# Performance work log

Hardware: AMD Instinct MI355X
Metric: run time of the kernel (lower is better)

Reference implementation:

```python
import jax, jax.numpy as jnp
import numpy as np
from jax import lax

DATA_NUM, CNUM, AUG_NUM, LNUM = 64, 6, 4, 3
B, H, W = 16, 512, 512
T_SEL = 0  # fixed aug selection (torch draws np.random.randint at runtime)
EPS = 1e-8
DN = ('NCHW', 'OIHW', 'NCHW')


def setup_inputs() -> dict:
    key = jax.random.key(0)
    ks = jax.random.split(key, 8)
    GLA_img_aug = jax.random.uniform(ks[0], (B, 1, H, W), dtype=jnp.float32)
    lbl = jax.random.randint(ks[1], (B, H, W), 0, CNUM, dtype=jnp.int32)
    index = jax.random.randint(ks[2], (B,), 0, DATA_NUM, dtype=jnp.int32)
    # learned params: Bezier control params (5+2=7 slots, only 0..3 used) and per-(sample,class,aug,layer) tiny conv pairs
    param = jax.random.uniform(ks[3], (DATA_NUM, CNUM, AUG_NUM, LNUM, 7), dtype=jnp.float32)
    w1 = 0.1 * jax.random.normal(ks[4], (DATA_NUM, CNUM, AUG_NUM, LNUM, 4, 1, 3, 3), dtype=jnp.float32)
    b1 = 0.01 * jax.random.normal(ks[5], (DATA_NUM, CNUM, AUG_NUM, LNUM, 4), dtype=jnp.float32)
    w2 = 0.1 * jax.random.normal(ks[6], (DATA_NUM, CNUM, AUG_NUM, LNUM, 1, 4, 3, 3), dtype=jnp.float32)
    b2 = 0.01 * jax.random.normal(ks[7], (DATA_NUM, CNUM, AUG_NUM, LNUM, 1), dtype=jnp.float32)
    return {"GLA_img_aug": GLA_img_aug, "lbl": lbl, "index": index,
            "param": param, "w1": w1, "b1": b1, "w2": w2, "b2": b2}


def _conv_pair(x, w1, b1, w2, b2):
    # x: [1,H,W]; per-sample Conv2d(1,4,3,p=1) -> Conv2d(4,1,3,p=1)
    y = lax.conv_general_dilated(x[None], w1, (1, 1), 'SAME', dimension_numbers=DN) + b1[None, :, None, None]
    y = lax.conv_general_dilated(y, w2, (1, 1), 'SAME', dimension_numbers=DN) + b2[None, :, None, None]
    return y[0]

_conv_batch = jax.vmap(_conv_pair)  # batched over per-sample weights


def _ftransfer(xn, lbl, i, index, param, w1, b1, w2, b2):
    raw = xn                                   # [B,1,H,W]
    mask = (lbl[:, None, :, :] == i)           # [B,1,H,W]
    c = xn * mask
    pp = jax.nn.sigmoid(param[index, i, T_SEL])   # [B,L,7]  (p := sigmoid)
    W1, B1 = w1[index, i, T_SEL], b1[index, i, T_SEL]
    W2, B2 = w2[index, i, T_SEL], b2[index, i, T_SEL]
    for layer in range(LNUM):
        p1 = pp[:, layer, 0][:, None, None, None]
        p2 = pp[:, layer, 1][:, None, None, None]
        p1v = pp[:, layer, 2][:, None, None, None]
        p2v = pp[:, layer, 3][:, None, None, None]
        mix = jax.nn.sigmoid(_conv_batch(raw, W1[:, layer], B1[:, layer], W2[:, layer], B2[:, layer]))
        om = 1.0 - c
        ct = 3.0 * om**2 * c * p1 + 3.0 * om * c**2 * p2 + c**3          # p0=0,  p3=1
        cv = om**3 + 3.0 * om**2 * c * p1v + 3.0 * om * c**2 * p2v       # p0v=1, p3v=0
        c = jnp.clip(ct * mix + cv * (1.0 - mix), 0.0, 1.0)
    # write back only where label == i (equivalent to torch's flag-filtered scatter)
    return jnp.where(mask, c, raw)


def reference(GLA_img_aug, lbl, index, param, w1, b1, w2, b2):
    x = GLA_img_aug
    mn = jnp.min(x, axis=(1, 2, 3), keepdims=True)
    mx = jnp.max(x, axis=(1, 2, 3), keepdims=True)
    scale = mx - mn + EPS
    xn = (x - mn) / scale
    for i in range(CNUM):
        xn = _ftransfer(xn, lbl, i, index, param, w1, b1, w2, b2)
    return xn * scale + mn
```

## Files before the change

kernel.cpp:

```cpp
#include <hip/hip_runtime.h>
#include <stdint.h>

#define HW 512
#define IMG (HW*HW)
#define CNUM_ 6

#define TILE 64
#define HALO 12
#define ST 88
#define SSTR 89
#define NT 512
#define RCAP 256

typedef float f2 __attribute__((ext_vector_type(2)));

#define LTOT 3840

#define RECBASE 2048
#define REC_F 96
#define VARBASE (RECBASE + 96*REC_F)
#define VAR_F 27

__global__ __launch_bounds__(256) void k_prep(const float4* __restrict__ x4,
                       const int* __restrict__ index, const float* __restrict__ param,
                       const float* __restrict__ w1, const float* __restrict__ b1,
                       const float* __restrict__ w2, const float* __restrict__ b2,
                       float* __restrict__ wsf){
    __shared__ float w1s[108], w2s[108], b1s[12], b2s[3], prm[21];
    __shared__ float smn[4], smx[4];
    const int r = blockIdx.x, t = threadIdx.x;
    if (r >= 96){
        int blk = r - 96;
        int base4 = blk * 1024;
        float vmin = 1e30f, vmax = -1e30f;
#pragma unroll
        for (int k = 0; k < 4; k++){
            float4 v = x4[base4 + k*256 + t];
            vmin = fminf(vmin, fminf(fminf(v.x, v.y), fminf(v.z, v.w)));
            vmax = fmaxf(vmax, fmaxf(fmaxf(v.x, v.y), fmaxf(v.z, v.w)));
        }
#pragma unroll
        for (int off = 32; off > 0; off >>= 1){
            vmin = fminf(vmin, __shfl_down(vmin, off));
            vmax = fmaxf(vmax, __shfl_down(vmax, off));
        }
        int wv = t >> 6;
        if ((t & 63) == 0){ smn[wv] = vmin; smx[wv] = vmax; }
        __syncthreads();
        if (t == 0){
            wsf[2*blk]     = fminf(fminf(smn[0], smn[1]), fminf(smn[2], smn[3]));
            wsf[2*blk + 1] = fmaxf(fmaxf(smx[0], smx[1]), fmaxf(smx[2], smx[3]));
        }
        return;
    }
    const int b = r / 6, i = r % 6;
    const int lb0 = (index[b]*CNUM_ + i) * 12;
    if (t < 108){
        int l = t / 36, j = t % 36;
        w1s[t] = w1[(lb0 + l)*36 + j];
        w2s[t] = w2[(lb0 + l)*36 + j];
    }
    if (t < 12) b1s[t] = b1[(lb0 + t/4)*4 + (t%4)];
    if (t < 3)  b2s[t] = b2[lb0 + t];
    if (t < 21) prm[t] = param[(lb0 + t/7)*7 + (t%7)];
    __syncthreads();
    float* rec = wsf + RECBASE + r*REC_F;
    float* var = wsf + VARBASE + r*9*3*VAR_F;
    for (int u = t; u < 9*3*26; u += 256){
        int kind = u / 78, rem = u % 78, l = rem / 26, e = rem % 26;
        int rowk = kind / 3, colk = kind % 3;
        if (e < 25){
            int ty = e/5 - 2, tx = e%5 - 2;
            float we = 0.f;
            for (int d = 0; d < 9; d++){
                int dy = d/3 - 1, dx = d%3 - 1;
                if ((rowk==0 && dy<0)||(rowk==2 && dy>0)||(colk==0 && dx<0)||(colk==2 && dx>0)) continue;
                int ey = ty - dy, ex = tx - dx;
                if (ey < -1 || ey > 1 || ex < -1 || ex > 1) continue;
                for (int c = 0; c < 4; c++)
                    we += w2s[l*36 + c*9 + d] * w1s[l*36 + c*9 + (ey+1)*3 + (ex+1)];
            }
            var[(kind*3 + l)*VAR_F + e] = we;
            if (kind == 4) rec[l*25 + e] = we;
        } else {
            float be = b2s[l];
            for (int c = 0; c < 4; c++){
                float sw = 0.f;
                for (int d = 0; d < 9; d++){
                    int dy = d/3 - 1, dx = d%3 - 1;
                    if ((rowk==0 && dy<0)||(rowk==2 && dy>0)||(colk==0 && dx<0)||(colk==2 && dx>0)) continue;
                    sw += w2s[l*36 + c*9 + d];
                }
                be += b1s[l*4 + c] * sw;
            }
            var[(kind*3 + l)*VAR_F + 25] = be;
            if (kind == 4) rec[75 + l] = be;
        }
    }
    if (t < 18){
        int l = t / 6, q = t % 6;
        float p1  = __builtin_amdgcn_rcpf(1.f + __expf(-prm[l*7 + 0]));
        float p2  = __builtin_amdgcn_rcpf(1.f + __expf(-prm[l*7 + 1]));
        float p1v = __builtin_amdgcn_rcpf(1.f + __expf(-prm[l*7 + 2]));
        float p2v = __builtin_amdgcn_rcpf(1.f + __expf(-prm[l*7 + 3]));
        float v;
        switch (q){
            case 0: v = 3.f*p1; break;
            case 1: v = 3.f*p2 - 6.f*p1; break;
            case 2: v = 1.f + 3.f*p1 - 3.f*p2; break;
            case 3: v = 3.f*p1v - 3.f; break;
            case 4: v = 3.f - 6.f*p1v + 3.f*p2v; break;
            default: v = -1.f + 3.f*p1v - 3.f*p2v; break;
        }
        rec[78 + l*6 + q] = v;
    }
}

__device__ __forceinline__ float sig1(float z){
    return __builtin_amdgcn_rcpf(1.f + __expf(-z));
}

__device__ __forceinline__ float bez3(float c, float mix, const float* __restrict__ cf){
    float ct = c * (cf[0] + c * (cf[1] + c * cf[2]));
    float cv = 1.f + c * (cf[3] + c * (cf[4] + c * cf[5]));
    float r = cv + mix * (ct - cv);
    return __builtin_amdgcn_fmed3f(r, 0.f, 1.f);
}

__device__ __forceinline__ f2 splat(float v){ f2 r = {v, v}; return r; }

__device__ __forceinline__ f2 sig2(f2 z){
    f2 r;
    r.x = __builtin_amdgcn_rcpf(1.f + __expf(-z.x));
    r.y = __builtin_amdgcn_rcpf(1.f + __expf(-z.y));
    return r;
}

__device__ __forceinline__ f2 bez3p(f2 c, f2 mix, const float* __restrict__ cf){
    f2 ct = c * (splat(cf[0]) + c * (splat(cf[1]) + c * splat(cf[2])));
    f2 cv = splat(1.f) + c * (splat(cf[3]) + c * (splat(cf[4]) + c * splat(cf[5])));
    f2 r = cv + mix * (ct - cv);
    r.x = __builtin_amdgcn_fmed3f(r.x, 0.f, 1.f);
    r.y = __builtin_amdgcn_fmed3f(r.y, 0.f, 1.f);
    return r;
}

__device__ __forceinline__ void load_taps(const float* __restrict__ s, int pos, float* tp){
    const float* sp0 = s + pos - (2*SSTR + 2);
    const float* sp1 = s + pos + (SSTR - 2);
#pragma unroll
    for (int wy = 0; wy < 3; wy++)
#pragma unroll
    for (int wx = 0; wx < 5; wx++)
        tp[wy*5 + wx] = sp0[wy*SSTR + wx];
#pragma unroll
    for (int wy = 0; wy < 2; wy++)
#pragma unroll
    for (int wx = 0; wx < 5; wx++)
        tp[15 + wy*5 + wx] = sp1[wy*SSTR + wx];
}

__device__ __forceinline__ void conv_px(const float* __restrict__ s, int pos,
                                        const float* __restrict__ rec,
                                        float& z0, float& z1, float& z2, float& cc){
    float tp[25];
    load_taps(s, pos, tp);
    f2 a0 = {rec[75], 0.f};
    f2 a1 = {rec[76], 0.f};
    f2 a2 = {rec[77], 0.f};
#pragma unroll
    for (int e = 0; e < 24; e += 2){
        f2 tv = {tp[e], tp[e+1]};
        f2 w0 = {rec[e],      rec[e+1]};
        f2 w1 = {rec[25 + e], rec[26 + e]};
        f2 w2 = {rec[50 + e], rec[51 + e]};
        a0 += w0 * tv;
        a1 += w1 * tv;
        a2 += w2 * tv;
    }
    float t24 = tp[24];
    z0 = a0.x + a0.y + rec[24]*t24;
    z1 = a1.x + a1.y + rec[49]*t24;
    z2 = a2.x + a2.y + rec[74]*t24;
    cc = tp[12];
}

__device__ __forceinline__ unsigned short* gl_addr(float* out, int sbase, int Y0, int X0, int e){
    return (unsigned short*)(out + sbase + (Y0 + HALO + (e >> 7))*HW + X0 + HALO) + (e & 127);
}

__device__ __forceinline__ void classify_px(int ce, unsigned short pos, int lane,
        int* cnt, unsigned short* lst, float* out, int sbase, int Y0, int X0){
    unsigned long long m0 = __ballot(ce & 1);
    unsigned long long m1 = __ballot(ce & 2);
    unsigned long long m2 = __ballot(ce & 4);
    int basev = 0;
    if (lane < 6){
        unsigned long long mc = ((lane & 1) ? m0 : ~m0)
                              & ((lane & 2) ? m1 : ~m1)
                              & ((lane & 4) ? m2 : ~m2);
        int pc = __popcll(mc);
        if (pc) basev = atomicAdd(&cnt[lane], pc);
    }
    int mybase = __shfl(basev, ce < 6 ? ce : 0);
    if (ce < 6){
        unsigned long long mself = ((ce & 1) ? m0 : ~m0)
                                 & ((ce & 2) ? m1 : ~m1)
                                 & ((ce & 4) ? m2 : ~m2);
        int p = mybase + __popcll(mself & ((1ull << lane) - 1ull));
        if (ce < 3){
            int capc = 1408 - (ce << 7);
            int offc = ce * (1472 - (ce << 6));
            if (p < capc) lst[offc + p] = pos;
        } else {
            int d = ce - 3;
            int capc = 1056 - 96*d;
            int offc = d * (1104 - 48*d);
            if (p < capc) *gl_addr(out, sbase, Y0, X0, offc + p) = pos;
        }
    }
}

__global__ __launch_bounds__(NT, 8) void k_main(
        const float* __restrict__ x, const int* __restrict__ lbl,
        float* __restrict__ out, const float* __restrict__ wsf){
    __shared__ float s[ST*SSTR];
    __shared__ unsigned short lst[LTOT];
    __shared__ unsigned rlst[RCAP];
    __shared__ int cnt[8];
    __shared__ float snorm[4];
    const int lin = ((blockIdx.z << 3) + blockIdx.y) * 8 + blockIdx.x;
    const int tile = ((lin & 7) << 7) + (lin >> 3);
    const int bz = tile >> 6, by = (tile >> 3) & 7, bx = tile & 7;
    const int b = bz;
    const int X0 = bx * TILE - HALO, Y0 = by * TILE - HALO;
    const int tid = threadIdx.x;
    const int lane = tid & 63;
    const int sbase = b * IMG;
    const bool edgeblk = (bx == 0) | (bx == 7) | (by == 0) | (by == 7);

    if (tid < 8) cnt[tid] = 0;
    if (tid < 64){
        float pmn = wsf[2*(b*64 + tid)];
        float pmx = wsf[2*(b*64 + tid) + 1];
#pragma unroll
        for (int off = 32; off > 0; off >>= 1){
            pmn = fminf(pmn, __shfl_down(pmn, off));
            pmx = fmaxf(pmx, __shfl_down(pmx, off));
        }
        if (tid == 0){
            float scv = pmx - pmn + 1e-8f;
            snorm[0] = pmn; snorm[1] = scv; snorm[2] = 1.0f / scv;
        }
    }
    __syncthreads();
    const float mn = snorm[0], sc = snorm[1], inv = snorm[2];
    const float mninv = mn * inv;

    if (!edgeblk){
        int q = tid << 2;
        int ly = q / ST, lx = q - ly*ST;
        int pbase = ly*SSTR + lx;
        for (int it = 0; it < 4; it++){
            bool act = (it < 3) | (tid < (ST*ST - 3*4*NT) / 4);
            float4 xv = {0.f, 0.f, 0.f, 0.f};
            int4  lv = {255, 255, 255, 255};
            if (act){
                int off = sbase + ((Y0 + ly) << 9) + (X0 + lx);
                xv = *(const float4*)(x + off);
                lv = *(const int4*)(lbl + off);
                s[pbase + 0] = xv.x*inv - mninv;
                s[pbase + 1] = xv.y*inv - mninv;
                s[pbase + 2] = xv.z*inv - mninv;
                s[pbase + 3] = xv.w*inv - mninv;
            }
            int mrow = min(ly, ST-1-ly);
#pragma unroll
            for (int j = 0; j < 4; j++){
                int c = (&lv.x)[j];
                int lxj = lx + j;
                int margin = min(min(lxj, ST-1-lxj), mrow);
                int ce = 7;
                if (act && c < CNUM_ && margin >= 2 + 2*c) ce = c;
                classify_px(ce, (unsigned short)(pbase + j), lane, cnt, lst, out, sbase, Y0, X0);
            }
            lx += 24; ly += 23; pbase += 23*SSTR + 24;
            if (lx >= ST){ lx -= ST; ly += 1; pbase += SSTR - ST; }
        }
    } else {
        int ly = tid / ST, lx = tid % ST;
        int pos = ly*SSTR + lx;
        for (int it = 0; it < 16; it++){
            bool inb = ly < ST;
            int gy = Y0 + ly, gx = X0 + lx;
            bool valid = inb && (unsigned)gy < (unsigned)HW && (unsigned)gx < (unsigned)HW;
            float v = 0.f; int c = 255;
            if (valid){
                int off = sbase + (gy << 9) + gx;
                v = x[off]*inv - mninv;
                c = lbl[off];
            }
            if (inb) s[pos] = v;
            int margin = min(min(lx, ST-1-lx), min(ly, ST-1-ly));
            bool ring = valid && ((gx==0) | (gx==HW-1) | (gy==0) | (gy==HW-1));
            bool mainok = valid && !ring && c < CNUM_ && margin >= 2 + 2*c;
            int ce = mainok ? c : 7;
            classify_px(ce, (unsigned short)pos, lane, cnt, lst, out, sbase, Y0, X0);
            {
                bool ringok = ring && c < CNUM_ && margin >= 2;
                unsigned long long rm = __ballot(ringok);
                if (rm){
                    int base = 0;
                    if (lane == 0) base = atomicAdd(&cnt[6], __popcll(rm));
                    base = __shfl(base, 0);
                    if (ringok){
                        int p = base + __popcll(rm & ((1ull << lane) - 1ull));
                        if (p < RCAP) rlst[p] = ((unsigned)c << 16) | (unsigned)pos;
                    }
                }
            }
            lx += 72; ly += 5; pos += 517;
            if (lx >= ST){ lx -= ST; ly += 1; pos += 1; }
        }
    }
    __syncthreads();
    const int rn = min(cnt[6], RCAP);

    unsigned short pf[9];
#pragma unroll
    for (int d = 0; d < 3; d++){
        int capc = 1056 - 96*d;
        int offc = d * (1104 - 48*d);
        int nB = min(cnt[3 + d], capc);
#pragma unroll
        for (int sl = 0; sl < 3; sl++){
            int j = tid + sl*NT;
            unsigned short pv = 0;
            if (j < nB) pv = *gl_addr(out, sbase, Y0, X0, offc + j);
            pf[d*3 + sl] = pv;
        }
    }

#pragma unroll
    for (int cls = 0; cls < CNUM_; cls++){
        const int capc = (cls < 3) ? (1408 - (cls << 7)) : (1056 - 96*(cls - 3));
        const float* rec = wsf + RECBASE + (b*CNUM_ + cls)*REC_F;
        const int n = min(cnt[cls], capc);
        const int j0 = tid, j1 = tid + NT, j2 = tid + 2*NT;
        const bool v0 = j0 < n, v1 = j1 < n, v2 = j2 < n;
        int p0 = 0, p1 = 0, p2 = 0;
        if (cls < 3){
            const unsigned short* lp = lst + cls * (1472 - (cls << 6));
            if (v0) p0 = lp[j0];
            if (v1) p1 = lp[j1];
            if (v2) p2 = lp[j2];
        } else {
            p0 = pf[(cls-3)*3 + 0];
            p1 = pf[(cls-3)*3 + 1];
            p2 = pf[(cls-3)*3 + 2];
        }
        __builtin_amdgcn_s_setprio(1);
        float z00=0.f, z01=0.f, z02=0.f, cc0=0.f;
        float z10=0.f, z11=0.f, z12=0.f, cc1=0.f;
        float u0, u1, u2;
        if (v0) conv_px(s, p0, rec, z00, z01, z02, cc0);
        if (v1) conv_px(s, p1, rec, z10, z11, z12, cc1);
        if (v0 | v1){
            f2 cP = {cc0, cc1};
            cP = bez3p(cP, sig2((f2){z00, z10}), rec + 78);
            cP = bez3p(cP, sig2((f2){z01, z11}), rec + 84);
            cP = bez3p(cP, sig2((f2){z02, z12}), rec + 90);
            u0 = cP.x; u1 = cP.y;
        }
        if (v2){
            float za, zb, zc, cc;
            conv_px(s, p2, rec, za, zb, zc, cc);
            cc = bez3(cc, sig1(za), rec + 78);
            cc = bez3(cc, sig1(zb), rec + 84);
            u2 = bez3(cc, sig1(zc), rec + 90);
        }
        __builtin_amdgcn_s_setprio(0);
        int hav = -1; float rupd = 0.f;
        if (edgeblk && tid < rn){
            unsigned e = rlst[tid];
            int rc = (int)(e >> 16), pos = (int)(e & 0xffff);
            int ly = pos / SSTR, lx = pos % SSTR;
            int margin = min(min(lx, ST-1-lx), min(ly, ST-1-ly));
            if (rc == cls && margin >= 2 + 2*cls){
                int gy = Y0 + ly, gx = X0 + lx;
                int rowk = (gy == 0) ? 0 : ((gy == HW-1) ? 2 : 1);
                int colk = (gx == 0) ? 0 : ((gx == HW-1) ? 2 : 1);
                const float* vb = wsf + VARBASE + ((b*CNUM_ + cls)*9 + rowk*3 + colk)*3*VAR_F;
                float tp[25];
                load_taps(s, pos, tp);
                float c = tp[12];
#pragma unroll
                for (int l = 0; l < 3; l++){
                    float z = vb[l*VAR_F + 25];
#pragma unroll
                    for (int e2 = 0; e2 < 25; e2++) z += vb[l*VAR_F + e2] * tp[e2];
                    c = bez3(c, sig1(z), rec + 78 + 6*l);
                }
                rupd = c; hav = pos;
            }
        }
        __syncthreads();
        if (v0) s[p0] = u0;
        if (v1) s[p1] = u1;
        if (v2) s[p2] = u2;
        if (hav >= 0) s[hav] = rupd;
        __syncthreads();
    }

    for (int j = tid; j < TILE*TILE; j += NT){
        int py = j >> 6, px = j & 63;
        int gy = Y0 + HALO + py, gx = X0 + HALO + px;
        out[sbase + gy*HW + gx] = s[(HALO + py)*SSTR + (HALO + px)] * sc + mn;
    }
}

extern "C" void kernel_launch(void* const* d_in, const int* in_sizes, int n_in,
                              void* d_out, int out_size, void* d_ws, size_t ws_size,
                              hipStream_t stream){
    const float* x     = (const float*)d_in[0];
    const int*   lbl   = (const int*)  d_in[1];
    const int*   index = (const int*)  d_in[2];
    const float* param = (const float*)d_in[3];
    const float* w1    = (const float*)d_in[4];
    const float* b1    = (const float*)d_in[5];
    const float* w2    = (const float*)d_in[6];
    const float* b2    = (const float*)d_in[7];
    float* out = (float*)d_out;
    float* wsf = (float*)d_ws;

    k_prep<<<1120, 256, 0, stream>>>((const float4*)x, index, param, w1, b1, w2, b2, wsf);
    dim3 g(8, 8, 16);
    k_main<<<g, NT, 0, stream>>>(x, lbl, out, wsf);
}
```

Baseline: 165.8 us.

## Remap tiles so each XCD owns two images; vectorize edge-block loads

The block-to-tile mapping is rewritten so each XCD (lin&7) handles two whole images, and edge tiles are scheduled first, before interior tiles. This is meant to improve L2 locality of halo reads and to balance the slower edge blocks. Edge blocks now share the float4/int4 vectorized load path with interior blocks, using per-quad bounds checks in place of the scalar 16-iteration loop. The risk is that quads straddling the image boundary rely on X0 alignment to be handled correctly.

```diff
diff --git a/kernel.cpp b/kernel.cpp
--- a/kernel.cpp
+++ b/kernel.cpp
@@ -230,9 +230,20 @@
     __shared__ int cnt[8];
     __shared__ float snorm[4];
     const int lin = ((blockIdx.z << 3) + blockIdx.y) * 8 + blockIdx.x;
-    const int tile = ((lin & 7) << 7) + (lin >> 3);
-    const int bz = tile >> 6, by = (tile >> 3) & 7, bx = tile & 7;
-    const int b = bz;
+    const int xcd = lin & 7;
+    const int e = lin >> 3;
+    int img2, idx;
+    if (e < 56){
+        int r = e >> 1; img2 = e & 1;
+        if (r < 8)       idx = r;
+        else if (r < 16) idx = 56 + (r - 8);
+        else { int t = r - 16; idx = (1 + (t >> 1))*8 + (t & 1)*7; }
+    } else {
+        int f = e - 56; img2 = f & 1; int t = f >> 1;
+        idx = (1 + t/6)*8 + 1 + t%6;
+    }
+    const int b = xcd*2 + img2;
+    const int by = idx >> 3, bx = idx & 7;
     const int X0 = bx * TILE - HALO, Y0 = by * TILE - HALO;
     const int tid = threadIdx.x;
     const int lane = tid & 63;
@@ -257,22 +268,30 @@
     const float mn = snorm[0], sc = snorm[1], inv = snorm[2];
     const float mninv = mn * inv;
 
-    if (!edgeblk){
+    {
         int q = tid << 2;
         int ly = q / ST, lx = q - ly*ST;
         int pbase = ly*SSTR + lx;
         for (int it = 0; it < 4; it++){
             bool act = (it < 3) | (tid < (ST*ST - 3*4*NT) / 4);
+            int gy = Y0 + ly, gxb = X0 + lx;
+            bool vq = act & ((unsigned)gy < (unsigned)HW) & ((unsigned)gxb <= (unsigned)(HW - 4));
             float4 xv = {0.f, 0.f, 0.f, 0.f};
             int4  lv = {255, 255, 255, 255};
-            if (act){
-                int off = sbase + ((Y0 + ly) << 9) + (X0 + lx);
+            if (vq){
+                int off = sbase + (gy << 9) + gxb;
                 xv = *(const float4*)(x + off);
                 lv = *(const int4*)(lbl + off);
-                s[pbase + 0] = xv.x*inv - mninv;
-                s[pbase + 1] = xv.y*inv - mninv;
-                s[pbase + 2] = xv.z*inv - mninv;
-                s[pbase + 3] = xv.w*inv - mninv;
+                xv.x = xv.x*inv - mninv;
+                xv.y = xv.y*inv - mninv;
+                xv.z = xv.z*inv - mninv;
+                xv.w = xv.w*inv - mninv;
+            }
+            if (act){
+                s[pbase + 0] = xv.x;
+                s[pbase + 1] = xv.y;
+                s[pbase + 2] = xv.z;
+                s[pbase + 3] = xv.w;
             }
             int mrow = min(ly, ST-1-ly);
 #pragma unroll
@@ -280,47 +299,29 @@
                 int c = (&lv.x)[j];
                 int lxj = lx + j;
                 int margin = min(min(lxj, ST-1-lxj), mrow);
-                int ce = 7;
-                if (act && c < CNUM_ && margin >= 2 + 2*c) ce = c;
+                bool ringj = false;
+                if (edgeblk){
+                    int gxj = gxb + j;
+                    ringj = vq & ((gxj==0) | (gxj==HW-1) | (gy==0) | (gy==HW-1));
+                }
+                int ce = (c < CNUM_ && !ringj && margin >= 2 + 2*c) ? c : 7;
                 classify_px(ce, (unsigned short)(pbase + j), lane, cnt, lst, out, sbase, Y0, X0);
+                if (edgeblk){
+                    bool ringok = ringj && c < CNUM_ && margin >= 2;
+                    unsigned long long rm = __ballot(ringok);
+                    if (rm){
+                        int base = 0;
+                        if (lane == 0) base = atomicAdd(&cnt[6], __popcll(rm));
+                        base = __shfl(base, 0);
+                        if (ringok){
+                            int p = base + __popcll(rm & ((1ull << lane) - 1ull));
+                            if (p < RCAP) rlst[p] = ((unsigned)c << 16) | (unsigned)(pbase + j);
+                        }
+                    }
+                }
             }
             lx += 24; ly += 23; pbase += 23*SSTR + 24;
             if (lx >= ST){ lx -= ST; ly += 1; pbase += SSTR - ST; }
-        }
-    } else {
-        int ly = tid / ST, lx = tid % ST;
-        int pos = ly*SSTR + lx;
-        for (int it = 0; it < 16; it++){
-            bool inb = ly < ST;
-            int gy = Y0 + ly, gx = X0 + lx;
-            bool valid = inb && (unsigned)gy < (unsigned)HW && (unsigned)gx < (unsigned)HW;
-            float v = 0.f; int c = 255;
-            if (valid){
-                int off = sbase + (gy << 9) + gx;
-                v = x[off]*inv - mninv;
-                c = lbl[off];
-            }
-            if (inb) s[pos] = v;
-            int margin = min(min(lx, ST-1-lx), min(ly, ST-1-ly));
-            bool ring = valid && ((gx==0) | (gx==HW-1) | (gy==0) | (gy==HW-1));
-            bool mainok = valid && !ring && c < CNUM_ && margin >= 2 + 2*c;
-            int ce = mainok ? c : 7;
-            classify_px(ce, (unsigned short)pos, lane, cnt, lst, out, sbase, Y0, X0);
-            {
-                bool ringok = ring && c < CNUM_ && margin >= 2;
-                unsigned long long rm = __ballot(ringok);
-                if (rm){
-                    int base = 0;
-                    if (lane == 0) base = atomicAdd(&cnt[6], __popcll(rm));
-                    base = __shfl(base, 0);
-                    if (ringok){
-                        int p = base + __popcll(rm & ((1ull << lane) - 1ull));
-                        if (p < RCAP) rlst[p] = ((unsigned)c << 16) | (unsigned)pos;
-                    }
-                }
-            }
-            lx += 72; ly += 5; pos += 517;
-            if (lx >= ST){ lx -= ST; ly += 1; pos += 1; }
         }
     }
     __syncthreads();
@@ -382,8 +383,8 @@
         __builtin_amdgcn_s_setprio(0);
         int hav = -1; float rupd = 0.f;
         if (edgeblk && tid < rn){
-            unsigned e = rlst[tid];
-            int rc = (int)(e >> 16), pos = (int)(e & 0xffff);
+            unsigned ev = rlst[tid];
+            int rc = (int)(ev >> 16), pos = (int)(ev & 0xffff);
             int ly = pos / SSTR, lx = pos % SSTR;
             int margin = min(min(lx, ST-1-lx), min(ly, ST-1-ly));
             if (rc == cls && margin >= 2 + 2*cls){
```

Result: no change. 164.1 us (-1.0%).
